# Kernel tuning notes

Measured on AMD Instinct MI355X. Metric: run time of the kernel, lower is better.

The kernel has to match this reference:

```python
import jax, jax.numpy as jnp
import numpy as np

VAR_NUM = [29, 2, 1, 6, 7, 59, 1, 24, 76, 711, 3, 9, 1]  # sums to 929
TEMP = 0.8
EPS = 1e-20


def setup_inputs() -> dict:
    key = jax.random.key(0)
    ks = jax.random.split(key, 8)
    B, D, H, O = 32768, 128, 1024, 929
    s = lambda n: 1.0 / np.sqrt(n)
    return {
        "x": jax.random.normal(ks[0], (B, D), jnp.float32),
        "W1": jax.random.uniform(ks[1], (D, H), jnp.float32, -s(D), s(D)),
        "b1": jax.random.uniform(ks[2], (H,), jnp.float32, -s(D), s(D)),
        "W2": jax.random.uniform(ks[3], (H, H), jnp.float32, -s(H), s(H)),
        "b2": jax.random.uniform(ks[4], (H,), jnp.float32, -s(H), s(H)),
        "W3": jax.random.uniform(ks[5], (H, O), jnp.float32, -s(H), s(H)),
        "b3": jax.random.uniform(ks[6], (O,), jnp.float32, -s(H), s(H)),
        "u": jax.random.uniform(ks[7], (B, O), jnp.float32),  # U(0,1) gumbel base noise
    }


def reference(x, W1, b1, W2, b2, W3, b3, u):
    h = jax.nn.elu(x @ W1 + b1)          # [B, H]
    h = jax.nn.sigmoid(h @ W2 + b2)      # [B, H]
    logits = h @ W3 + b3                 # [B, 929]
    g = -jnp.log(-jnp.log(u + EPS) + EPS)  # gumbel noise, [B, 929]
    outs = []
    off = 0
    for n in VAR_NUM:  # fixed 13 segments
        seg = logits[:, off:off + n]
        if n == 1:
            outs.append(seg)  # passthrough for continuous columns
        else:
            y = (seg + g[:, off:off + n]) / TEMP
            outs.append(jax.nn.softmax(y, axis=-1))
        off += n
    return jnp.concatenate(outs, axis=1)  # [B, 929]
```

## Files before the change

### kernel.cpp

```cpp
#include <hip/hip_runtime.h>
#include <hip/hip_bf16.h>
#include <stdint.h>

#define GEPS 1e-20f

typedef __bf16 bf16x8 __attribute__((ext_vector_type(8)));
typedef float  f32x4  __attribute__((ext_vector_type(4)));

typedef const __attribute__((address_space(1))) uint32_t* gptr32;
typedef __attribute__((address_space(3))) uint32_t* lptr32;

__device__ __forceinline__ void load_lds16(const void* g, void* l) {
    __builtin_amdgcn_global_load_lds((gptr32)g, (lptr32)l, 16, 0, 0);
}

__device__ __forceinline__ uint16_t f2bf(float v) {
    __hip_bfloat16 b = __float2bfloat16(v);
    return *(uint16_t*)&b;
}
__device__ __forceinline__ float bf2f(uint16_t b) {
    uint32_t u = (uint32_t)b << 16;
    return __builtin_bit_cast(float, u);
}

#define LN2   0.69314718056f
#define LOG2E 1.44269504089f
__device__ __forceinline__ float fast_log(float x) { return __builtin_amdgcn_logf(x) * LN2; }
__device__ __forceinline__ float fast_exp(float x) { return __builtin_amdgcn_exp2f(x * LOG2E); }
__device__ __forceinline__ float fast_exp2(float x) { return __builtin_amdgcn_exp2f(x); }
__device__ __forceinline__ float fast_rcp(float x)  { return __builtin_amdgcn_rcpf(x); }

__device__ __forceinline__ void store_val(uint16_t* C, size_t idx, float v) { C[idx] = f2bf(v); }
__device__ __forceinline__ void store_val(float* C, size_t idx, float v)    { C[idx] = v; }

__global__ void cast_bf16(const float* __restrict__ in, uint16_t* __restrict__ out, int n) {
    int i = (blockIdx.x * blockDim.x + threadIdx.x) * 4;
    if (i < n) {
        float4 v = *(const float4*)(in + i);
        ushort4 o;
        o.x = f2bf(v.x); o.y = f2bf(v.y); o.z = f2bf(v.z); o.w = f2bf(v.w);
        *(ushort4*)(out + i) = o;
    }
}

__global__ void transpose_cast(const float* __restrict__ W, uint16_t* __restrict__ Wt,
                               int K, int N, int Npad) {
    __shared__ float tile[64][65];
    const int k0 = blockIdx.y * 64, n0 = blockIdx.x * 64;
    const int tx = threadIdx.x & 63, ty = threadIdx.x >> 6;
    for (int r = ty; r < 64; r += 4) {
        int n = n0 + tx;
        tile[r][tx] = (n < N) ? W[(size_t)(k0 + r) * N + n] : 0.f;
    }
    __syncthreads();
    for (int r = ty; r < 64; r += 4) {
        Wt[(size_t)(n0 + r) * K + k0 + tx] = f2bf(tile[tx][r]);
    }
}

template<int ACT, typename OutT, bool SNG>
__global__ __launch_bounds__(256)
void gemm_bt(const uint16_t* __restrict__ A, const uint16_t* __restrict__ Bt,
             const float* __restrict__ bias, OutT* __restrict__ C,
             float* __restrict__ sngl,
             int K, int Nout, int ldc) {
    __shared__ __align__(16) uint16_t As[128 * 32];
    __shared__ __align__(16) uint16_t Bs[128 * 32];

    const int t    = threadIdx.x;
    const int wave = t >> 6, lane = t & 63;

    const int nbx = gridDim.x;
    const int bid = blockIdx.y * nbx + blockIdx.x;
    const int xcd = bid & 7;
    const int s   = bid >> 3;
    const int nidx = s % nbx;
    const int midx = xcd * (gridDim.y >> 3) + s / nbx;

    const int m0 = midx * 128, n0 = nidx * 128;
    const int wm = (wave >> 1) * 64, wn = (wave & 1) * 64;
    const int quad = lane >> 4;
    const int qk   = quad * 8;
    const int r15  = lane & 15;

    f32x4 acc[4][4] = {};

    const uint16_t* Ag = A  + (size_t)m0 * K;
    const uint16_t* Bg = Bt + (size_t)n0 * K;

    for (int k0 = 0; k0 < K; k0 += 32) {
        __syncthreads();
        #pragma unroll
        for (int rd = 0; rd < 2; ++rd) {
            int c = t + rd * 256;
            int row = c >> 2, kc = (c & 3) * 8;
            load_lds16(Ag + (size_t)row * K + k0 + kc, &As[c * 8]);
            load_lds16(Bg + (size_t)row * K + k0 + kc, &Bs[c * 8]);
        }
        __syncthreads();

        bf16x8 a[4], b[4];
        #pragma unroll
        for (int i = 0; i < 4; ++i)
            a[i] = *(const bf16x8*)&As[(wm + i * 16 + r15) * 32 + qk];
        #pragma unroll
        for (int i = 0; i < 4; ++i)
            b[i] = *(const bf16x8*)&Bs[(wn + i * 16 + r15) * 32 + qk];

        #pragma unroll
        for (int mi = 0; mi < 4; ++mi)
            #pragma unroll
            for (int ni = 0; ni < 4; ++ni)
                acc[mi][ni] = __builtin_amdgcn_mfma_f32_16x16x32_bf16(
                    a[mi], b[ni], acc[mi][ni], 0, 0, 0);
    }

    #pragma unroll
    for (int ni = 0; ni < 4; ++ni) {
        int col = n0 + wn + ni * 16 + r15;
        if (col < Nout) {
            float bv = bias[col];
            bool is_sng = SNG && (col == 31 || col == 104 || col == 928);
            #pragma unroll
            for (int mi = 0; mi < 4; ++mi) {
                #pragma unroll
                for (int r = 0; r < 4; ++r) {
                    int row = m0 + wm + mi * 16 + quad * 4 + r;
                    float v = acc[mi][ni][r] + bv;
                    if (ACT == 1) v = (v > 0.f) ? v : (fast_exp(v) - 1.f);
                    else if (ACT == 2) v = fast_rcp(1.f + fast_exp(-v));
                    store_val(C, (size_t)row * ldc + col, v);
                    if constexpr (SNG) {
                        if (is_sng) sngl[(size_t)row * 929 + col] = v;
                    }
                }
            }
        }
    }
}

#define BARRIER() asm volatile("s_barrier" ::: "memory")
#define LGKM0()   asm volatile("s_waitcnt lgkmcnt(0)" ::: "memory")
#define VMW4()    asm volatile("s_waitcnt vmcnt(4)" ::: "memory")
#define VMW0()    asm volatile("s_waitcnt vmcnt(0)" ::: "memory")
#define PRIO1()   __builtin_amdgcn_s_setprio(1)
#define PRIO0()   __builtin_amdgcn_s_setprio(0)

template<int ACT, typename OutT, bool SNG, int K>
__global__ __launch_bounds__(512, 2)
void gemm256(const uint16_t* __restrict__ A, const uint16_t* __restrict__ Bt,
             const float* __restrict__ bias, OutT* __restrict__ C,
             float* __restrict__ sngl, int Nout, int ldc) {
    constexpr int NT = K / 64;
    constexpr int NI = NT / 2;
    constexpr int KB = K * 2;
    __shared__ __align__(16) char lds[131072];
    constexpr int AOFF0 = 0, BOFF0 = 32768, AOFF1 = 65536, BOFF1 = 98304;

    const int t = threadIdx.x;
    const int wave = t >> 6, lane = t & 63;
    const int quad = lane >> 4, r15 = lane & 15;
    const int wm = (wave >> 2) * 128, wn = (wave & 3) * 64;

    const int nbx = gridDim.x;
    const int bid = blockIdx.y * nbx + blockIdx.x;
    const int xcd = bid & 7;
    const int sb  = bid >> 3;
    const int nidx = sb % nbx;
    const int midx = xcd * (gridDim.y >> 3) + sb / nbx;
    const int m0 = midx * 256, n0 = nidx * 256;

    const int srow = t >> 3;
    const int scb  = ((t & 7) ^ (srow & 7)) << 4;
    const char* Asrc = (const char*)A  + (size_t)(m0 + srow) * KB + scb;
    const char* Bsrc = (const char*)Bt + (size_t)(n0 + srow) * KB + scb;

    const int sx   = (r15 & 7) << 4;
    const int cb0  = (quad * 16) ^ sx;
    const int cb1  = (64 + quad * 16) ^ sx;
    const int aRow = (wm + r15) * 128;
    const int bRow = (wn + r15) * 128;

    f32x4 acc[8][4] = {};
    bf16x8 a[4][2], b[4][2];

#define STG(src, half, tile, ldsOff)                                                      \
    do {                                                                                  \
        const char* _s = (src) + (size_t)((half) * 128) * KB + (size_t)(tile) * 128;      \
        load_lds16(_s,                   &lds[(ldsOff) + (half) * 16384 + t * 16]);       \
        load_lds16(_s + (size_t)64 * KB, &lds[(ldsOff) + (half) * 16384 + 8192 + t * 16]);\
    } while (0)

    auto ldA = [&](int buf, int mh) {
        #pragma unroll
        for (int mi = 0; mi < 4; ++mi) {
            const int base = buf * 65536 + aRow + (mh * 4 + mi) * 2048;
            a[mi][0] = *(const bf16x8*)&lds[base + cb0];
            a[mi][1] = *(const bf16x8*)&lds[base + cb1];
        }
    };
    auto ldB = [&](int buf, int nh) {
        #pragma unroll
        for (int ni = 0; ni < 2; ++ni) {
            const int base = buf * 65536 + 32768 + bRow + (nh * 2 + ni) * 2048;
            b[nh * 2 + ni][0] = *(const bf16x8*)&lds[base + cb0];
            b[nh * 2 + ni][1] = *(const bf16x8*)&lds[base + cb1];
        }
    };
    auto mfmaQ = [&](int mlo, int nlo) {
        #pragma unroll
        for (int mi = 0; mi < 4; ++mi)
            #pragma unroll
            for (int ni = 0; ni < 2; ++ni)
                #pragma unroll
                for (int kk = 0; kk < 2; ++kk)
                    acc[mlo + mi][nlo + ni] = __builtin_amdgcn_mfma_f32_16x16x32_bf16(
                        a[mi][kk], b[nlo + ni][kk], acc[mlo + mi][nlo + ni], 0, 0, 0);
    };

    STG(Bsrc, 0, 0, BOFF0); STG(Bsrc, 1, 0, BOFF0);
    STG(Asrc, 0, 0, AOFF0); STG(Asrc, 1, 0, AOFF0);
    STG(Bsrc, 0, 1, BOFF1); STG(Bsrc, 1, 1, BOFF1);
    VMW4(); BARRIER();

    #pragma unroll 1
    for (int ki = 0; ki < NI; ++ki) {
        const int t1 = 2 * ki + 1;
        const int p0 = (2 * ki + 2) & (NT - 1);
        const int p1 = (2 * ki + 3) & (NT - 1);

        ldA(0, 0); ldB(0, 0);
        STG(Asrc, 0, t1, AOFF1);
        BARRIER();
        PRIO1(); mfmaQ(0, 0); PRIO0();
        LGKM0(); BARRIER();

        ldB(0, 1);
        STG(Asrc, 1, t1, AOFF1);
        BARRIER();
        PRIO1(); mfmaQ(0, 2); PRIO0();
        LGKM0(); BARRIER();

        ldA(0, 1);
        STG(Bsrc, 0, p0, BOFF0);
        BARRIER();
        PRIO1(); mfmaQ(4, 2); PRIO0();
        LGKM0(); BARRIER();

        STG(Bsrc, 1, p0, BOFF0);
        BARRIER();
        PRIO1(); mfmaQ(4, 0); PRIO0();
        VMW4(); BARRIER();

        ldA(1, 0); ldB(1, 0);
        STG(Asrc, 0, p0, AOFF0);
        BARRIER();
        PRIO1(); mfmaQ(0, 0); PRIO0();
        LGKM0(); BARRIER();

        ldB(1, 1);
        STG(Asrc, 1, p0, AOFF0);
        BARRIER();
        PRIO1(); mfmaQ(0, 2); PRIO0();
        LGKM0(); BARRIER();

        ldA(1, 1);
        STG(Bsrc, 0, p1, BOFF1);
        BARRIER();
        PRIO1(); mfmaQ(4, 2); PRIO0();
        LGKM0(); BARRIER();

        STG(Bsrc, 1, p1, BOFF1);
        BARRIER();
        PRIO1(); mfmaQ(4, 0); PRIO0();
        VMW4(); BARRIER();
    }
    VMW0();

#undef STG

    #pragma unroll
    for (int ni = 0; ni < 4; ++ni) {
        const int col = n0 + wn + ni * 16 + r15;
        if (col < Nout) {
            const float bv = bias[col];
            const bool is_sng = SNG && (col == 31 || col == 104 || col == 928);
            #pragma unroll
            for (int mi = 0; mi < 8; ++mi) {
                #pragma unroll
                for (int r = 0; r < 4; ++r) {
                    const int row = m0 + wm + mi * 16 + quad * 4 + r;
                    float v = acc[mi][ni][r] + bv;
                    if (ACT == 1) v = (v > 0.f) ? v : (fast_exp(v) - 1.f);
                    else if (ACT == 2) v = fast_rcp(1.f + fast_exp(-v));
                    store_val(C, (size_t)row * ldc + col, v);
                    if constexpr (SNG) {
                        if (is_sng) sngl[(size_t)row * 929 + col] = v;
                    }
                }
            }
        }
    }
}

#define NEG_BIG (-1e30f)
#define Y2_LG   1.8033688011f

__device__ __forceinline__ float y2_col(const uint16_t* __restrict__ rlg,
                                        const float* __restrict__ ru, int c) {
    float l2u   = __builtin_amdgcn_logf(ru[c] + GEPS);
    float inner = fmaf(-LN2, l2u, GEPS);
    float l2i   = __builtin_amdgcn_logf(inner);
    return fmaf(Y2_LG, bf2f(rlg[c]), -1.25f * l2i);
}

template<int N, int OFF>
__device__ __forceinline__ void seg_small(const uint16_t* __restrict__ rlg,
                                          const float* __restrict__ ru,
                                          float* __restrict__ rout, int l32) {
    static_assert(N <= 32, "seg_small needs N<=32");
    constexpr int GS = (N <= 2) ? 2 : (N <= 4) ? 4 : (N <= 8) ? 8 : (N <= 16) ? 16 : 32;
    const bool act = l32 < N;
    const int  c   = OFF + l32;
    float y = act ? y2_col(rlg, ru, c) : NEG_BIG;
    float m = y;
    #pragma unroll
    for (int o = 1; o < GS; o <<= 1) m = fmaxf(m, __shfl_xor(m, o, 64));
    float e = act ? fast_exp2(y - m) : 0.f;
    float s = e;
    #pragma unroll
    for (int o = 1; o < GS; o <<= 1) s += __shfl_xor(s, o, 64);
    if (act) rout[c] = e * fast_rcp(s);
}

template<int N, int OFF>
__device__ __forceinline__ void seg_wide(const uint16_t* __restrict__ rlg,
                                         const float* __restrict__ ru,
                                         float* __restrict__ rout, int lane) {
    constexpr int IT = (N + 63) / 64;
    float y[IT];
    float m = NEG_BIG;
    #pragma unroll
    for (int i = 0; i < IT; ++i) {
        const int j = i * 64 + lane;
        y[i] = (j < N) ? y2_col(rlg, ru, OFF + j) : NEG_BIG;
        m = fmaxf(m, y[i]);
    }
    #pragma unroll
    for (int o = 1; o < 64; o <<= 1) m = fmaxf(m, __shfl_xor(m, o, 64));
    float s = 0.f;
    #pragma unroll
    for (int i = 0; i < IT; ++i) {
        float e = fast_exp2(y[i] - m);
        y[i] = e;
        s += e;
    }
    #pragma unroll
    for (int o = 1; o < 64; o <<= 1) s += __shfl_xor(s, o, 64);
    const float inv = fast_rcp(s);
    #pragma unroll
    for (int i = 0; i < IT; ++i) {
        const int j = i * 64 + lane;
        if (j < N) rout[OFF + j] = y[i] * inv;
    }
}

__global__ __launch_bounds__(256)
void gumbel_epilogue(const uint16_t* __restrict__ lg, float* __restrict__ out,
                     const float* __restrict__ u, int B) {
    const int wave = threadIdx.x >> 6, lane = threadIdx.x & 63;
    const int l32  = lane & 31, half = lane >> 5;
    const int rowA = blockIdx.x * 8 + wave * 2;
    if (rowA >= B) return;

    const size_t baseA = (size_t)rowA * 929;
    const size_t baseB = baseA + 929;
    const size_t baseH = half ? baseB : baseA;

    const uint16_t* lgH = lg  + baseH;
    const float*    uH  = u   + baseH;
    float*          oH  = out + baseH;
    seg_small<29,   0>(lgH, uH, oH, l32);
    seg_small< 2,  29>(lgH, uH, oH, l32);
    seg_small< 6,  32>(lgH, uH, oH, l32);
    seg_small< 7,  38>(lgH, uH, oH, l32);
    seg_small<24, 105>(lgH, uH, oH, l32);
    seg_small< 3, 916>(lgH, uH, oH, l32);
    seg_small< 9, 919>(lgH, uH, oH, l32);

    const uint16_t* lgA = lg + baseA; const float* uA = u + baseA; float* oA = out + baseA;
    const uint16_t* lgB = lg + baseB; const float* uB = u + baseB; float* oB = out + baseB;
    seg_wide< 59,  45>(lgA, uA, oA, lane);
    seg_wide< 59,  45>(lgB, uB, oB, lane);
    seg_wide< 76, 129>(lgA, uA, oA, lane);
    seg_wide< 76, 129>(lgB, uB, oB, lane);
    seg_wide<711, 205>(lgA, uA, oA, lane);
    seg_wide<711, 205>(lgB, uB, oB, lane);
}

extern "C" void kernel_launch(void* const* d_in, const int* in_sizes, int n_in,
                              void* d_out, int out_size, void* d_ws, size_t ws_size,
                              hipStream_t stream) {
    const float* x  = (const float*)d_in[0];
    const float* W1 = (const float*)d_in[1];
    const float* b1 = (const float*)d_in[2];
    const float* W2 = (const float*)d_in[3];
    const float* b2 = (const float*)d_in[4];
    const float* W3 = (const float*)d_in[5];
    const float* b3 = (const float*)d_in[6];
    const float* u  = (const float*)d_in[7];
    float* out = (float*)d_out;

    const int B = 32768, D = 128, H = 1024, O = 929, OP = 1024;

    char* ws = (char*)d_ws;
    uint16_t* xb  = (uint16_t*)ws; ws += (size_t)B * D * 2;
    uint16_t* w1t = (uint16_t*)ws; ws += (size_t)H * D * 2;
    uint16_t* w2t = (uint16_t*)ws; ws += (size_t)H * H * 2;
    uint16_t* w3t = (uint16_t*)ws; ws += (size_t)OP * H * 2;
    uint16_t* h1  = (uint16_t*)ws; ws += (size_t)B * H * 2;
    uint16_t* h2  = (uint16_t*)ws; ws += (size_t)B * H * 2;
    uint16_t* lg  = h1;

    cast_bf16<<<(B * D / 4 + 255) / 256, 256, 0, stream>>>(x, xb, B * D);
    transpose_cast<<<dim3(H / 64, D / 64), 256, 0, stream>>>(W1, w1t, D, H, H);
    transpose_cast<<<dim3(H / 64, H / 64), 256, 0, stream>>>(W2, w2t, H, H, H);
    transpose_cast<<<dim3(OP / 64, H / 64), 256, 0, stream>>>(W3, w3t, H, O, OP);

    gemm_bt<1, uint16_t, false><<<dim3(H / 128, B / 128), 256, 0, stream>>>(
        xb, w1t, b1, h1, nullptr, D, H, H);
    gemm256<2, uint16_t, false, 1024><<<dim3(H / 256, B / 256), 512, 0, stream>>>(
        h1, w2t, b2, h2, nullptr, H, H);
    gemm256<0, uint16_t, true, 1024><<<dim3(OP / 256, B / 256), 512, 0, stream>>>(
        h2, w3t, b3, lg, out, O, O);

    gumbel_epilogue<<<B / 8, 256, 0, stream>>>(lg, out, u, B);
}
```

Baseline: 484.8 us.

## Stage GEMM epilogue through swizzled LDS for coalesced stores; restructure prefetch schedule

The 256x256 GEMM epilogue now writes bf16 results into LDS with an XOR swizzle, then copies rows out with 16-byte coalesced vector stores. The logits buffer therefore uses a padded leading dimension of 1024, and the Gumbel epilogue indexing is updated to match. The main loop also issues the A-tile loads for the next stage earlier and in pairs, waiting at vmcnt(8) instead of vmcnt(4), which deepens in-flight global-to-LDS transfers. The costs are an extra LDS round-trip and barrier, and the larger ldc is written out to the full padded width.

```diff
diff --git a/kernel.cpp b/kernel.cpp
--- a/kernel.cpp
+++ b/kernel.cpp
@@ -141,7 +141,7 @@
 
 #define BARRIER() asm volatile("s_barrier" ::: "memory")
 #define LGKM0()   asm volatile("s_waitcnt lgkmcnt(0)" ::: "memory")
-#define VMW4()    asm volatile("s_waitcnt vmcnt(4)" ::: "memory")
+#define VMW8()    asm volatile("s_waitcnt vmcnt(8)" ::: "memory")
 #define VMW0()    asm volatile("s_waitcnt vmcnt(0)" ::: "memory")
 #define PRIO1()   __builtin_amdgcn_s_setprio(1)
 #define PRIO0()   __builtin_amdgcn_s_setprio(0)
@@ -221,84 +221,92 @@
     STG(Bsrc, 0, 0, BOFF0); STG(Bsrc, 1, 0, BOFF0);
     STG(Asrc, 0, 0, AOFF0); STG(Asrc, 1, 0, AOFF0);
     STG(Bsrc, 0, 1, BOFF1); STG(Bsrc, 1, 1, BOFF1);
-    VMW4(); BARRIER();
+    STG(Asrc, 0, 1, AOFF1); STG(Asrc, 1, 1, AOFF1);
+    VMW8(); BARRIER();
 
     #pragma unroll 1
     for (int ki = 0; ki < NI; ++ki) {
-        const int t1 = 2 * ki + 1;
         const int p0 = (2 * ki + 2) & (NT - 1);
         const int p1 = (2 * ki + 3) & (NT - 1);
 
         ldA(0, 0); ldB(0, 0);
-        STG(Asrc, 0, t1, AOFF1);
         BARRIER();
         PRIO1(); mfmaQ(0, 0); PRIO0();
         LGKM0(); BARRIER();
 
         ldB(0, 1);
-        STG(Asrc, 1, t1, AOFF1);
         BARRIER();
         PRIO1(); mfmaQ(0, 2); PRIO0();
         LGKM0(); BARRIER();
 
         ldA(0, 1);
-        STG(Bsrc, 0, p0, BOFF0);
+        STG(Bsrc, 0, p0, BOFF0); STG(Bsrc, 1, p0, BOFF0);
         BARRIER();
         PRIO1(); mfmaQ(4, 2); PRIO0();
         LGKM0(); BARRIER();
 
-        STG(Bsrc, 1, p0, BOFF0);
+        STG(Asrc, 0, p0, AOFF0); STG(Asrc, 1, p0, AOFF0);
         BARRIER();
         PRIO1(); mfmaQ(4, 0); PRIO0();
-        VMW4(); BARRIER();
+        VMW8(); BARRIER();
 
         ldA(1, 0); ldB(1, 0);
-        STG(Asrc, 0, p0, AOFF0);
         BARRIER();
         PRIO1(); mfmaQ(0, 0); PRIO0();
         LGKM0(); BARRIER();
 
         ldB(1, 1);
-        STG(Asrc, 1, p0, AOFF0);
         BARRIER();
         PRIO1(); mfmaQ(0, 2); PRIO0();
         LGKM0(); BARRIER();
 
         ldA(1, 1);
-        STG(Bsrc, 0, p1, BOFF1);
+        STG(Bsrc, 0, p1, BOFF1); STG(Bsrc, 1, p1, BOFF1);
         BARRIER();
         PRIO1(); mfmaQ(4, 2); PRIO0();
         LGKM0(); BARRIER();
 
-        STG(Bsrc, 1, p1, BOFF1);
+        STG(Asrc, 0, p1, AOFF1); STG(Asrc, 1, p1, AOFF1);
         BARRIER();
         PRIO1(); mfmaQ(4, 0); PRIO0();
-        VMW4(); BARRIER();
+        VMW8(); BARRIER();
     }
     VMW0();
+    BARRIER();
 
 #undef STG
 
     #pragma unroll
     for (int ni = 0; ni < 4; ++ni) {
-        const int col = n0 + wn + ni * 16 + r15;
-        if (col < Nout) {
-            const float bv = bias[col];
-            const bool is_sng = SNG && (col == 31 || col == 104 || col == 928);
+        const int col = wn + ni * 16 + r15;
+        const int gc  = n0 + col;
+        const float bv = (gc < Nout) ? bias[gc] : 0.f;
+        const bool is_sng = SNG && (gc == 31 || gc == 104 || gc == 928);
+        #pragma unroll
+        for (int mi = 0; mi < 8; ++mi) {
             #pragma unroll
-            for (int mi = 0; mi < 8; ++mi) {
-                #pragma unroll
-                for (int r = 0; r < 4; ++r) {
-                    const int row = m0 + wm + mi * 16 + quad * 4 + r;
-                    float v = acc[mi][ni][r] + bv;
-                    if (ACT == 1) v = (v > 0.f) ? v : (fast_exp(v) - 1.f);
-                    else if (ACT == 2) v = fast_rcp(1.f + fast_exp(-v));
-                    store_val(C, (size_t)row * ldc + col, v);
-                    if constexpr (SNG) {
-                        if (is_sng) sngl[(size_t)row * 929 + col] = v;
-                    }
+            for (int r = 0; r < 4; ++r) {
+                const int row = wm + mi * 16 + quad * 4 + r;
+                float v = acc[mi][ni][r] + bv;
+                if (ACT == 1) v = (v > 0.f) ? v : (fast_exp(v) - 1.f);
+                else if (ACT == 2) v = fast_rcp(1.f + fast_exp(-v));
+                *(uint16_t*)&lds[row * 512 + ((col * 2) ^ ((row & 7) << 4))] = f2bf(v);
+                if constexpr (SNG) {
+                    if (is_sng) sngl[(size_t)(m0 + row) * 929 + gc] = v;
                 }
             }
+        }
+    }
+    LGKM0(); BARRIER();
+
+    {
+        const int rt = t >> 5;
+        const int cc = t & 31;
+        #pragma unroll 1
+        for (int pass = 0; pass < 16; ++pass) {
+            const int row = pass * 16 + rt;
+            f32x4 v4 = *(const f32x4*)&lds[row * 512 + ((cc * 16) ^ ((row & 7) << 4))];
+            *(f32x4*)&C[(size_t)(m0 + row) * ldc + n0 + cc * 8] = v4;
         }
     }
 }
@@ -373,13 +381,16 @@
     const int rowA = blockIdx.x * 8 + wave * 2;
     if (rowA >= B) return;
 
-    const size_t baseA = (size_t)rowA * 929;
-    const size_t baseB = baseA + 929;
-    const size_t baseH = half ? baseB : baseA;
-
-    const uint16_t* lgH = lg  + baseH;
-    const float*    uH  = u   + baseH;
-    float*          oH  = out + baseH;
+    const size_t uoA  = (size_t)rowA * 929;
+    const size_t uoB  = uoA + 929;
+    const size_t lgoA = (size_t)rowA * 1024;
+    const size_t lgoB = lgoA + 1024;
+    const size_t uoH  = half ? uoB  : uoA;
+    const size_t lgoH = half ? lgoB : lgoA;
+
+    const uint16_t* lgH = lg  + lgoH;
+    const float*    uH  = u   + uoH;
+    float*          oH  = out + uoH;
     seg_small<29,   0>(lgH, uH, oH, l32);
     seg_small< 2,  29>(lgH, uH, oH, l32);
     seg_small< 6,  32>(lgH, uH, oH, l32);
@@ -388,8 +399,8 @@
     seg_small< 3, 916>(lgH, uH, oH, l32);
     seg_small< 9, 919>(lgH, uH, oH, l32);
 
-    const uint16_t* lgA = lg + baseA; const float* uA = u + baseA; float* oA = out + baseA;
-    const uint16_t* lgB = lg + baseB; const float* uB = u + baseB; float* oB = out + baseB;
+    const uint16_t* lgA = lg + lgoA; const float* uA = u + uoA; float* oA = out + uoA;
+    const uint16_t* lgB = lg + lgoB; const float* uB = u + uoB; float* oB = out + uoB;
     seg_wide< 59,  45>(lgA, uA, oA, lane);
     seg_wide< 59,  45>(lgB, uB, oB, lane);
     seg_wide< 76, 129>(lgA, uA, oA, lane);
@@ -432,7 +443,7 @@
     gemm256<2, uint16_t, false, 1024><<<dim3(H / 256, B / 256), 512, 0, stream>>>(
         h1, w2t, b2, h2, nullptr, H, H);
     gemm256<0, uint16_t, true, 1024><<<dim3(OP / 256, B / 256), 512, 0, stream>>>(
-        h2, w3t, b3, lg, out, O, O);
+        h2, w3t, b3, lg, out, O, 1024);
 
     gumbel_epilogue<<<B / 8, 256, 0, stream>>>(lg, out, u, B);
 }
```

Result: faster. 463.7 us (-4.3%).
